# Kernel tuning notes

Hardware: AMD Instinct MI355X
Metric: run time of the kernel (lower is better)

Reference implementation:

```python
import math
import jax, jax.numpy as jnp
import numpy as np

B, H, SQ, SK, D, M = 2, 16, 2048, 2048, 128, 128

def setup_inputs() -> dict:
    key = jax.random.key(0)
    kq, kk, ks = jax.random.split(key, 3)
    q = jax.random.normal(kq, (B, H, SQ, D), dtype=jnp.float32)
    k = jax.random.normal(kk, (B, H, SK, D), dtype=jnp.float32)
    # Gaussian projection matrix S of shape (m, dim), as in generate_projection_matrix
    S = jax.random.normal(ks, (M, D), dtype=jnp.float32)
    return {"q": q, "k": k, "S": S}


def reference(q, k, S):
    """QJL: quantize keys to sign bits + norm, then asymmetric inner-product estimate.

    quantize(k):  sign_bits = sign(k @ S.T) with sign(0) -> +1;  norm_k = ||k||_2
    estimate:     <q,k> ~= <S q, sign(S k)> * (sqrt(pi/2)/m) * ||k||
    """
    m = S.shape[0]
    scale = np.float32(math.sqrt(math.pi / 2.0)) / np.float32(m)
    # --- quantize keys ---
    norm_k = jnp.linalg.norm(k, axis=-1)                      # (B,H,SK)
    proj_k = jnp.einsum('bhkd,md->bhkm', k, S)                # (B,H,SK,M)
    sign_bits = jnp.where(proj_k >= 0, 1.0, -1.0).astype(jnp.float32)
    # --- project queries (asymmetric, no quantization) ---
    Sq = jnp.einsum('bhqd,md->bhqm', q, S)                    # (B,H,SQ,M)
    # --- estimate inner products: (Sq * signs).sum(-1) for every (q, k) pair ---
    dots = jnp.einsum('bhqm,bhkm->bhqk', Sq, sign_bits)       # (B,H,SQ,SK)
    estimated = dots * scale * norm_k[:, :, None, :]
    return estimated
```

## Files before the change

kernel.cpp:

```cpp
#include <hip/hip_runtime.h>
#include <hip/hip_bf16.h>
#include <math.h>

#define NBH   32
#define SEQ   2048
#define DD    128
#define MM    128

typedef unsigned short u16;
typedef unsigned int   u32;
typedef unsigned char  u8;
typedef float  f32x4  __attribute__((ext_vector_type(4)));
typedef __bf16 bf16x8 __attribute__((ext_vector_type(8)));

#define SCALE_F 0.009791516697777346f
#define TAU 0.18f
#define CCAP 2048

static __device__ __forceinline__ u16 f2bf(float f) {
  union { float f; u32 u; } v; v.f = f;
  u32 u = v.u;
  u += 0x7fffu + ((u >> 16) & 1u);
  return (u16)(u >> 16);
}

static __device__ __forceinline__ u32 f64_negbit(const float* __restrict__ K,
                                                 const float* __restrict__ S,
                                                 int row_g, int m) {
  const f32x4* kr = (const f32x4*)(K + (size_t)row_g * DD);
  const f32x4* sr = (const f32x4*)(S + (size_t)m * DD);
  double a0 = 0, a1 = 0, a2 = 0, a3 = 0;
#pragma unroll
  for (int d = 0; d < 32; d += 4) {
    f32x4 x0 = kr[d],   y0 = sr[d];
    f32x4 x1 = kr[d+1], y1 = sr[d+1];
    f32x4 x2 = kr[d+2], y2 = sr[d+2];
    f32x4 x3 = kr[d+3], y3 = sr[d+3];
    a0 += (double)x0.x*y0.x + (double)x0.y*y0.y + (double)x0.z*y0.z + (double)x0.w*y0.w;
    a1 += (double)x1.x*y1.x + (double)x1.y*y1.y + (double)x1.z*y1.z + (double)x1.w*y1.w;
    a2 += (double)x2.x*y2.x + (double)x2.y*y2.y + (double)x2.z*y2.z + (double)x2.w*y2.w;
    a3 += (double)x3.x*y3.x + (double)x3.y*y3.y + (double)x3.z*y3.z + (double)x3.w*y3.w;
  }
  return (((a0 + a1) + (a2 + a3)) < 0.0) ? 1u : 0u;
}

static __device__ __forceinline__ void mfma_tile(const u16* lA, const u16* lB,
                                                 int wave, int lane,
                                                 f32x4 acc[4][4]) {
  const int wr = wave >> 1, wc = wave & 1;
  const int lrow = lane & 15, lkg = lane >> 4;
#pragma unroll
  for (int kk = 0; kk < 4; ++kk) {
    bf16x8 af[4], bfr[4];
    const int c = kk * 4 + lkg;
#pragma unroll
    for (int a = 0; a < 4; ++a) {
      const int r  = wr * 64 + a * 16 + lrow;
      const int r2 = wc * 64 + a * 16 + lrow;
      af[a]  = *(const bf16x8*)((const char*)lA + r  * 256 + ((c ^ (r  & 7)) << 4));
      bfr[a] = *(const bf16x8*)((const char*)lB + r2 * 256 + ((c ^ (r2 & 7)) << 4));
    }
#pragma unroll
    for (int a = 0; a < 4; ++a)
#pragma unroll
      for (int b = 0; b < 4; ++b)
        acc[a][b] = __builtin_amdgcn_mfma_f32_16x16x32_bf16(af[a], bfr[b], acc[a][b], 0, 0, 0);
  }
}

static __device__ __forceinline__ void stage_f32_to_bf16(const float* __restrict__ src,
                                                         u16* lds, int tid) {
#pragma unroll
  for (int j = 0; j < 8; ++j) {
    int i = tid + j * 256;
    int r = i >> 4, c = i & 15;
    const f32x4* gp = (const f32x4*)(src + (size_t)r * DD + c * 8);
    f32x4 v0 = gp[0], v1 = gp[1];
    union { u16 h[8]; f32x4 v; } pk;
    pk.h[0] = f2bf(v0.x); pk.h[1] = f2bf(v0.y); pk.h[2] = f2bf(v0.z); pk.h[3] = f2bf(v0.w);
    pk.h[4] = f2bf(v1.x); pk.h[5] = f2bf(v1.y); pk.h[6] = f2bf(v1.z); pk.h[7] = f2bf(v1.w);
    *(f32x4*)((char*)lds + r * 256 + ((c ^ (r & 7)) << 4)) = pk.v;
  }
}

__global__ __launch_bounds__(256) void k_proj(
    const float* __restrict__ Q, const float* __restrict__ K,
    const float* __restrict__ S, u16* __restrict__ Sqb, u8* __restrict__ Sgb,
    float* __restrict__ sn) {
  __shared__ __align__(16) u16 lds2[2 * 128 * 128];
  __shared__ u16 cbuf[CCAP];
  __shared__ u32 lcnt;
  u16* lA = lds2;
  u16* lB = lds2 + 128 * 128;
  const int tid = threadIdx.x;
  const int tile = blockIdx.x;
  const bool isK = (tile >= 512);
  const int row0 = (isK ? (tile - 512) : tile) * 128;
  const float* src = isK ? K : Q;

  if (tid == 0) lcnt = 0;

  stage_f32_to_bf16(S, lB, tid);
  stage_f32_to_bf16(src + (size_t)row0 * DD, lA, tid);

  if (isK) {
    const int row = tid >> 1, half = tid & 1;
    const f32x4* base = (const f32x4*)(src + (size_t)(row0 + row) * DD) + half * 16;
    float s = 0.f;
#pragma unroll
    for (int j = 0; j < 16; ++j) {
      f32x4 v = base[j];
      s += v.x * v.x + v.y * v.y + v.z * v.z + v.w * v.w;
    }
    s += __shfl_xor(s, 1);
    if (half == 0) sn[row0 + row] = SCALE_F * sqrtf(s);
  }
  __syncthreads();

  const int wave = tid >> 6, lane = tid & 63;
  f32x4 acc[4][4];
#pragma unroll
  for (int a = 0; a < 4; ++a)
#pragma unroll
    for (int b = 0; b < 4; ++b) acc[a][b] = (f32x4){0.f, 0.f, 0.f, 0.f};

  mfma_tile(lA, lB, wave, lane, acc);

  __syncthreads();
  float* lc = (float*)lds2;
  const int wr = wave >> 1, wc = wave & 1;
#pragma unroll
  for (int a = 0; a < 4; ++a) {
#pragma unroll
    for (int b = 0; b < 4; ++b) {
      const int col = wc * 64 + b * 16 + (lane & 15);
#pragma unroll
      for (int j = 0; j < 4; ++j) {
        const int row = wr * 64 + a * 16 + (lane >> 4) * 4 + j;
        lc[row * 128 + (col ^ (((row >> 2) & 1) << 4))] = acc[a][b][j];
      }
    }
  }
  __syncthreads();

  const int c8 = tid & 15;
  const int rr = tid >> 4;
#pragma unroll
  for (int p = 0; p < 8; ++p) {
    const int row = rr + p * 16;
    const int s = (row >> 2) & 1;
    const int cb = (c8 ^ (s << 1)) * 8;
    f32x4 v0 = *(const f32x4*)&lc[row * 128 + cb];
    f32x4 v1 = *(const f32x4*)&lc[row * 128 + cb + 4];
    float vals[8] = {v0.x, v0.y, v0.z, v0.w, v1.x, v1.y, v1.z, v1.w};
    const int row_g = row0 + row;
    if (!isK) {
      union { u16 h[8]; f32x4 v; } pk;
#pragma unroll
      for (int e = 0; e < 8; ++e) pk.h[e] = f2bf(vals[e]);
      *(f32x4*)(Sqb + (size_t)row_g * MM + c8 * 8) = pk.v;
    } else {
      u32 byteval = 0;
#pragma unroll
      for (int e = 0; e < 8; ++e) {
        const int m = c8 * 8 + e;
        u32 bitneg = (vals[e] < 0.f) ? 1u : 0u;
        if (fabsf(vals[e]) < TAU) {
          u32 pos = atomicAdd(&lcnt, 1u);
          if (pos < CCAP) cbuf[pos] = (u16)((row << 8) | (bitneg << 7) | m);
          else bitneg = f64_negbit(K, S, row_g, m);
        }
        byteval |= bitneg << e;
      }
      Sgb[(size_t)row_g * 16 + c8] = (u8)byteval;
    }
  }

  if (isK) {
    __syncthreads();
    __threadfence();
    u32 n = lcnt; if (n > CCAP) n = CCAP;
    u32* Sg32 = (u32*)Sgb;
    for (u32 i = tid; i < n; i += 256) {
      u32 code = cbuf[i];
      int r = (code >> 8) & 127, m = code & 127;
      u32 prov = (code >> 7) & 1;
      u32 f64b = f64_negbit(K, S, row0 + r, m);
      if (f64b != prov)
        atomicXor(Sg32 + (size_t)(row0 + r) * 4 + (m >> 5), 1u << (m & 31));
    }
  }
}

__global__ __launch_bounds__(256, 4) void k_gemm(
    const u16* __restrict__ Sqb, const u8* __restrict__ Sgb,
    const float* __restrict__ sn, float* __restrict__ out) {
  __shared__ __align__(16) char smem[32768 + 2048];
  const u32* lBb = (const u32*)(smem + 32768);
  const int tid = threadIdx.x;
  const u32 id = blockIdx.x;
  const u32 l = (id & 7) * 1024 + (id >> 3);
  const int tn = l & 15, tm = (l >> 4) & 15, bh = l >> 8;
  const char* Abase = (const char*)(Sqb + ((size_t)bh * SEQ + tm * 128) * MM);
  const char* Bbase = (const char*)(Sgb + ((size_t)bh * SEQ + tn * 128) * 16);

  {
    typedef __attribute__((address_space(3))) char lds_t;
    typedef const __attribute__((address_space(1))) char glob_t;
    const int wv = tid >> 6, ln = tid & 63;
#pragma unroll
    for (int j = 0; j < 8; ++j) {
      const int s = j * 256 + wv * 64 + ln;
      const int r = s >> 4, cp = s & 15;
      const int srcoff = r * 256 + ((cp ^ (r & 7)) << 4);
      __builtin_amdgcn_global_load_lds((glob_t*)(Abase + srcoff),
                                       (lds_t*)(smem + s * 16), 16, 0, 0);
    }
    if (tid < 128)
      __builtin_amdgcn_global_load_lds((glob_t*)(Bbase + tid * 16),
                                       (lds_t*)(smem + 32768 + tid * 16), 16, 0, 0);
  }
  __syncthreads();

  const int wave = tid >> 6, lane = tid & 63;
  const int wr = wave >> 1, wc = wave & 1;
  const int lrow = lane & 15, lkg = lane >> 4;
  f32x4 acc[4][4];
#pragma unroll
  for (int a = 0; a < 4; ++a)
#pragma unroll
    for (int b = 0; b < 4; ++b) acc[a][b] = (f32x4){0.f, 0.f, 0.f, 0.f};

#pragma unroll
  for (int kk = 0; kk < 4; ++kk) {
    const int c = kk * 4 + lkg;
    bf16x8 af[4], bfr[4];
#pragma unroll
    for (int a = 0; a < 4; ++a) {
      const int r = wr * 64 + a * 16 + lrow;
      af[a] = *(const bf16x8*)(smem + r * 256 + ((c ^ (r & 7)) << 4));
      const int r2 = wc * 64 + a * 16 + lrow;
      u32 word = lBb[r2 * 4 + kk];
      u32 byte = (word >> (lkg * 8)) & 0xFFu;
      union { u16 h[8]; bf16x8 v; } ub;
#pragma unroll
      for (int e = 0; e < 8; ++e) ub.h[e] = ((byte >> e) & 1u) ? 0xBF80 : 0x3F80;
      bfr[a] = ub.v;
    }
#pragma unroll
    for (int a = 0; a < 4; ++a)
#pragma unroll
      for (int b = 0; b < 4; ++b)
        acc[a][b] = __builtin_amdgcn_mfma_f32_16x16x32_bf16(af[a], bfr[b], acc[a][b], 0, 0, 0);
  }

  const float* snb = sn + bh * SEQ + tn * 128;
  const size_t outbase = (size_t)bh * SEQ * SEQ + (size_t)tm * 128 * SEQ + tn * 128;
  const int cch = tid & 31;
  const int hr0 = tid >> 5;
  const f32x4 s4 = *(const f32x4*)(snb + cch * 4);
  float* lc = (float*)smem;

#pragma unroll
  for (int h = 0; h < 2; ++h) {
    __syncthreads();
#pragma unroll
    for (int a2 = 0; a2 < 2; ++a2) {
      const int a = 2 * h + a2;
#pragma unroll
      for (int b = 0; b < 4; ++b) {
        const int col = wc * 64 + b * 16 + (lane & 15);
#pragma unroll
        for (int j = 0; j < 4; ++j) {
          const int hr = wr * 32 + a2 * 16 + (lane >> 4) * 4 + j;
          lc[hr * 128 + (col ^ (((hr >> 2) & 1) << 4))] = acc[a][b][j];
        }
      }
    }
    __syncthreads();
#pragma unroll
    for (int p = 0; p < 8; ++p) {
      const int hr = hr0 + p * 8;
      const int row = ((hr >> 5) << 6) + 32 * h + (hr & 31);
      const int cs = cch ^ (((hr >> 2) & 1) << 2);
      f32x4 v = *(const f32x4*)&lc[hr * 128 + cs * 4];
      v = v * s4;
      __builtin_nontemporal_store(v, (f32x4*)(out + outbase + (size_t)row * SEQ + cch * 4));
    }
  }
}

extern "C" void kernel_launch(void* const* d_in, const int* in_sizes, int n_in,
                              void* d_out, int out_size, void* d_ws, size_t ws_size,
                              hipStream_t stream) {
  const float* q = (const float*)d_in[0];
  const float* k = (const float*)d_in[1];
  const float* S = (const float*)d_in[2];
  float* out = (float*)d_out;
  char* ws = (char*)d_ws;

  const size_t off_Sq  = 0;
  const size_t off_Sg  = 16777216;
  const size_t off_sn  = 17825792;

  u16*   Sqb = (u16*)(ws + off_Sq);
  u8*    Sgb = (u8*)(ws + off_Sg);
  float* sn  = (float*)(ws + off_sn);

  k_proj<<<1024, 256, 0, stream>>>(q, k, S, Sqb, Sgb, sn);
  k_gemm<<<8192, 256, 0, stream>>>(Sqb, Sgb, sn, out);
}
```

Baseline: 163.0 us.

## Split projection kernel into half-M blocks with pre-converted bf16 S

```diff
diff --git a/kernel.cpp b/kernel.cpp
--- a/kernel.cpp
+++ b/kernel.cpp
@@ -2,7 +2,6 @@
 #include <hip/hip_bf16.h>
 #include <math.h>
 
-#define NBH   32
 #define SEQ   2048
 #define DD    128
 #define MM    128
@@ -15,7 +14,7 @@
 
 #define SCALE_F 0.009791516697777346f
 #define TAU 0.18f
-#define CCAP 2048
+#define CCAP 1024
 
 static __device__ __forceinline__ u16 f2bf(float f) {
   union { float f; u32 u; } v; v.f = f;
@@ -44,126 +43,119 @@
   return (((a0 + a1) + (a2 + a3)) < 0.0) ? 1u : 0u;
 }
 
-static __device__ __forceinline__ void mfma_tile(const u16* lA, const u16* lB,
-                                                 int wave, int lane,
-                                                 f32x4 acc[4][4]) {
-  const int wr = wave >> 1, wc = wave & 1;
+__global__ __launch_bounds__(256) void k_convS(const float* __restrict__ S,
+                                               u16* __restrict__ Sb) {
+  int i = blockIdx.x * 256 + threadIdx.x;
+  Sb[i] = f2bf(S[i]);
+}
+
+__global__ __launch_bounds__(256, 4) void k_proj(
+    const float* __restrict__ Q, const float* __restrict__ K,
+    const float* __restrict__ S, const u16* __restrict__ Sb,
+    u16* __restrict__ Sqb, u8* __restrict__ Sgb, float* __restrict__ sn) {
+  __shared__ __align__(16) char smem[32768];
+  __shared__ u16 cbuf[CCAP];
+  __shared__ u32 lcnt;
+  const int tid = threadIdx.x;
+  const u32 id = blockIdx.x;
+  const int mhalf = id & 1;
+  const bool isK = (id >> 1) & 1;
+  const int row0 = (int)(id >> 2) * 128;
+  const int col0 = mhalf * 64;
+  const float* src = isK ? K : Q;
+
+  if (tid == 0) lcnt = 0;
+
+  {
+    const bool donorm = isK && (mhalf == 0);
+#pragma unroll
+    for (int j = 0; j < 8; ++j) {
+      const int i = tid + j * 256;
+      const int r = i >> 4, c = i & 15;
+      const f32x4* gp = (const f32x4*)(src + (size_t)(row0 + r) * DD + c * 8);
+      f32x4 v0 = gp[0], v1 = gp[1];
+      union { u16 h[8]; f32x4 v; } pk;
+      pk.h[0] = f2bf(v0.x); pk.h[1] = f2bf(v0.y); pk.h[2] = f2bf(v0.z); pk.h[3] = f2bf(v0.w);
+      pk.h[4] = f2bf(v1.x); pk.h[5] = f2bf(v1.y); pk.h[6] = f2bf(v1.z); pk.h[7] = f2bf(v1.w);
+      *(f32x4*)(smem + r * 256 + ((c ^ (r & 7)) << 4)) = pk.v;
+      if (donorm) {
+        float ss = v0.x*v0.x + v0.y*v0.y + v0.z*v0.z + v0.w*v0.w
+                 + v1.x*v1.x + v1.y*v1.y + v1.z*v1.z + v1.w*v1.w;
+        ss += __shfl_xor(ss, 1); ss += __shfl_xor(ss, 2);
+        ss += __shfl_xor(ss, 4); ss += __shfl_xor(ss, 8);
+        if ((tid & 15) == 0) sn[row0 + r] = SCALE_F * sqrtf(ss);
+      }
+    }
+  }
+  __syncthreads();
+
+  const int wave = tid >> 6, lane = tid & 63;
   const int lrow = lane & 15, lkg = lane >> 4;
+  f32x4 acc[2][4];
+#pragma unroll
+  for (int a = 0; a < 2; ++a)
+#pragma unroll
+    for (int b = 0; b < 4; ++b) acc[a][b] = (f32x4){0.f, 0.f, 0.f, 0.f};
+
+  const char* Sbb = (const char*)Sb;
 #pragma unroll
   for (int kk = 0; kk < 4; ++kk) {
-    bf16x8 af[4], bfr[4];
     const int c = kk * 4 + lkg;
-#pragma unroll
-    for (int a = 0; a < 4; ++a) {
-      const int r  = wr * 64 + a * 16 + lrow;
-      const int r2 = wc * 64 + a * 16 + lrow;
-      af[a]  = *(const bf16x8*)((const char*)lA + r  * 256 + ((c ^ (r  & 7)) << 4));
-      bfr[a] = *(const bf16x8*)((const char*)lB + r2 * 256 + ((c ^ (r2 & 7)) << 4));
-    }
-#pragma unroll
-    for (int a = 0; a < 4; ++a)
+    bf16x8 af[2], bfr[4];
+#pragma unroll
+    for (int a = 0; a < 2; ++a) {
+      const int r = wave * 32 + a * 16 + lrow;
+      af[a] = *(const bf16x8*)(smem + r * 256 + ((c ^ (r & 7)) << 4));
+    }
+#pragma unroll
+    for (int b = 0; b < 4; ++b) {
+      const int r2 = col0 + b * 16 + lrow;
+      bfr[b] = *(const bf16x8*)(Sbb + (size_t)r2 * 256 + c * 16);
+    }
+#pragma unroll
+    for (int a = 0; a < 2; ++a)
 #pragma unroll
       for (int b = 0; b < 4; ++b)
         acc[a][b] = __builtin_amdgcn_mfma_f32_16x16x32_bf16(af[a], bfr[b], acc[a][b], 0, 0, 0);
   }
-}
-
-static __device__ __forceinline__ void stage_f32_to_bf16(const float* __restrict__ src,
-                                                         u16* lds, int tid) {
-#pragma unroll
-  for (int j = 0; j < 8; ++j) {
-    int i = tid + j * 256;
-    int r = i >> 4, c = i & 15;
-    const f32x4* gp = (const f32x4*)(src + (size_t)r * DD + c * 8);
-    f32x4 v0 = gp[0], v1 = gp[1];
-    union { u16 h[8]; f32x4 v; } pk;
-    pk.h[0] = f2bf(v0.x); pk.h[1] = f2bf(v0.y); pk.h[2] = f2bf(v0.z); pk.h[3] = f2bf(v0.w);
-    pk.h[4] = f2bf(v1.x); pk.h[5] = f2bf(v1.y); pk.h[6] = f2bf(v1.z); pk.h[7] = f2bf(v1.w);
-    *(f32x4*)((char*)lds + r * 256 + ((c ^ (r & 7)) << 4)) = pk.v;
-  }
-}
-
-__global__ __launch_bounds__(256) void k_proj(
-    const float* __restrict__ Q, const float* __restrict__ K,
-    const float* __restrict__ S, u16* __restrict__ Sqb, u8* __restrict__ Sgb,
-    float* __restrict__ sn) {
-  __shared__ __align__(16) u16 lds2[2 * 128 * 128];
-  __shared__ u16 cbuf[CCAP];
-  __shared__ u32 lcnt;
-  u16* lA = lds2;
-  u16* lB = lds2 + 128 * 128;
-  const int tid = threadIdx.x;
-  const int tile = blockIdx.x;
-  const bool isK = (tile >= 512);
-  const int row0 = (isK ? (tile - 512) : tile) * 128;
-  const float* src = isK ? K : Q;
-
-  if (tid == 0) lcnt = 0;
-
-  stage_f32_to_bf16(S, lB, tid);
-  stage_f32_to_bf16(src + (size_t)row0 * DD, lA, tid);
-
-  if (isK) {
-    const int row = tid >> 1, half = tid & 1;
-    const f32x4* base = (const f32x4*)(src + (size_t)(row0 + row) * DD) + half * 16;
-    float s = 0.f;
-#pragma unroll
-    for (int j = 0; j < 16; ++j) {
-      f32x4 v = base[j];
-      s += v.x * v.x + v.y * v.y + v.z * v.z + v.w * v.w;
-    }
-    s += __shfl_xor(s, 1);
-    if (half == 0) sn[row0 + row] = SCALE_F * sqrtf(s);
-  }
+
   __syncthreads();
-
-  const int wave = tid >> 6, lane = tid & 63;
-  f32x4 acc[4][4];
-#pragma unroll
-  for (int a = 0; a < 4; ++a)
-#pragma unroll
-    for (int b = 0; b < 4; ++b) acc[a][b] = (f32x4){0.f, 0.f, 0.f, 0.f};
-
-  mfma_tile(lA, lB, wave, lane, acc);
-
+  float* lc = (float*)smem;
+#pragma unroll
+  for (int a = 0; a < 2; ++a) {
+#pragma unroll
+    for (int b = 0; b < 4; ++b) {
+      const int col = b * 16 + (lane & 15);
+#pragma unroll
+      for (int j = 0; j < 4; ++j) {
+        const int row = wave * 32 + a * 16 + (lane >> 4) * 4 + j;
+        lc[row * 64 + (col ^ (((row >> 2) & 3) << 4))] = acc[a][b][j];
+      }
+    }
+  }
   __syncthreads();
-  float* lc = (float*)lds2;
-  const int wr = wave >> 1, wc = wave & 1;
-#pragma unroll
-  for (int a = 0; a < 4; ++a) {
-#pragma unroll
-    for (int b = 0; b < 4; ++b) {
-      const int col = wc * 64 + b * 16 + (lane & 15);
-#pragma unroll
-      for (int j = 0; j < 4; ++j) {
-        const int row = wr * 64 + a * 16 + (lane >> 4) * 4 + j;
-        lc[row * 128 + (col ^ (((row >> 2) & 1) << 4))] = acc[a][b][j];
-      }
-    }
-  }
-  __syncthreads();
-
-  const int c8 = tid & 15;
-  const int rr = tid >> 4;
-#pragma unroll
-  for (int p = 0; p < 8; ++p) {
-    const int row = rr + p * 16;
-    const int s = (row >> 2) & 1;
-    const int cb = (c8 ^ (s << 1)) * 8;
-    f32x4 v0 = *(const f32x4*)&lc[row * 128 + cb];
-    f32x4 v1 = *(const f32x4*)&lc[row * 128 + cb + 4];
+
+#pragma unroll
+  for (int it = 0; it < 4; ++it) {
+    const int ch = tid + it * 256;
+    const int row = ch >> 3, co = ch & 7;
+    const int sw = (row >> 2) & 3;
+    const int cq0 = (co * 2) ^ (sw << 2);
+    const int cq1 = (co * 2 + 1) ^ (sw << 2);
+    f32x4 v0 = *(const f32x4*)&lc[row * 64 + cq0 * 4];
+    f32x4 v1 = *(const f32x4*)&lc[row * 64 + cq1 * 4];
     float vals[8] = {v0.x, v0.y, v0.z, v0.w, v1.x, v1.y, v1.z, v1.w};
     const int row_g = row0 + row;
     if (!isK) {
       union { u16 h[8]; f32x4 v; } pk;
 #pragma unroll
       for (int e = 0; e < 8; ++e) pk.h[e] = f2bf(vals[e]);
-      *(f32x4*)(Sqb + (size_t)row_g * MM + c8 * 8) = pk.v;
+      *(f32x4*)(Sqb + (size_t)row_g * MM + col0 + co * 8) = pk.v;
     } else {
       u32 byteval = 0;
 #pragma unroll
       for (int e = 0; e < 8; ++e) {
-        const int m = c8 * 8 + e;
+        const int m = col0 + co * 8 + e;
         u32 bitneg = (vals[e] < 0.f) ? 1u : 0u;
         if (fabsf(vals[e]) < TAU) {
           u32 pos = atomicAdd(&lcnt, 1u);
@@ -172,7 +164,7 @@
         }
         byteval |= bitneg << e;
       }
-      Sgb[(size_t)row_g * 16 + c8] = (u8)byteval;
+      Sgb[(size_t)row_g * 16 + (col0 >> 3) + co] = (u8)byteval;
     }
   }
 
@@ -302,11 +294,14 @@
   const size_t off_Sq  = 0;
   const size_t off_Sg  = 16777216;
   const size_t off_sn  = 17825792;
+  const size_t off_Sb  = 18087936;
 
   u16*   Sqb = (u16*)(ws + off_Sq);
   u8*    Sgb = (u8*)(ws + off_Sg);
   float* sn  = (float*)(ws + off_sn);
-
-  k_proj<<<1024, 256, 0, stream>>>(q, k, S, Sqb, Sgb, sn);
+  u16*   Sb  = (u16*)(ws + off_Sb);
+
+  k_convS<<<64, 256, 0, stream>>>(S, Sb);
+  k_proj<<<2048, 256, 0, stream>>>(q, k, S, Sb, Sqb, Sgb, sn);
   k_gemm<<<8192, 256, 0, stream>>>(Sqb, Sgb, sn, out);
 }
```

After: 301.5 us. 85.0% more time.

## Prepack S into MFMA fragment layout and halve k_proj LDS footprint

Applied to the files above, without the earlier changes.

```diff
diff --git a/kernel.cpp b/kernel.cpp
--- a/kernel.cpp
+++ b/kernel.cpp
@@ -44,30 +44,6 @@
   return (((a0 + a1) + (a2 + a3)) < 0.0) ? 1u : 0u;
 }
 
-static __device__ __forceinline__ void mfma_tile(const u16* lA, const u16* lB,
-                                                 int wave, int lane,
-                                                 f32x4 acc[4][4]) {
-  const int wr = wave >> 1, wc = wave & 1;
-  const int lrow = lane & 15, lkg = lane >> 4;
-#pragma unroll
-  for (int kk = 0; kk < 4; ++kk) {
-    bf16x8 af[4], bfr[4];
-    const int c = kk * 4 + lkg;
-#pragma unroll
-    for (int a = 0; a < 4; ++a) {
-      const int r  = wr * 64 + a * 16 + lrow;
-      const int r2 = wc * 64 + a * 16 + lrow;
-      af[a]  = *(const bf16x8*)((const char*)lA + r  * 256 + ((c ^ (r  & 7)) << 4));
-      bfr[a] = *(const bf16x8*)((const char*)lB + r2 * 256 + ((c ^ (r2 & 7)) << 4));
-    }
-#pragma unroll
-    for (int a = 0; a < 4; ++a)
-#pragma unroll
-      for (int b = 0; b < 4; ++b)
-        acc[a][b] = __builtin_amdgcn_mfma_f32_16x16x32_bf16(af[a], bfr[b], acc[a][b], 0, 0, 0);
-  }
-}
-
 static __device__ __forceinline__ void stage_f32_to_bf16(const float* __restrict__ src,
                                                          u16* lds, int tid) {
 #pragma unroll
@@ -83,15 +59,27 @@
   }
 }
 
+__global__ __launch_bounds__(256) void k_packS(const float* __restrict__ S,
+                                               u16* __restrict__ Sf) {
+  const int b = blockIdx.x;
+  const int tid = threadIdx.x;
+  const int kk = tid >> 6, lane = tid & 63;
+  const int rl = lane & 15, g = lane >> 4;
+  const f32x4* gp = (const f32x4*)(S + (size_t)(b * 16 + rl) * DD + kk * 32 + g * 8);
+  f32x4 v0 = gp[0], v1 = gp[1];
+  union { u16 h[8]; f32x4 v; } pk;
+  pk.h[0] = f2bf(v0.x); pk.h[1] = f2bf(v0.y); pk.h[2] = f2bf(v0.z); pk.h[3] = f2bf(v0.w);
+  pk.h[4] = f2bf(v1.x); pk.h[5] = f2bf(v1.y); pk.h[6] = f2bf(v1.z); pk.h[7] = f2bf(v1.w);
+  *(f32x4*)(Sf + ((size_t)(b * 4 + kk) * 64 + lane) * 8) = pk.v;
+}
+
 __global__ __launch_bounds__(256) void k_proj(
     const float* __restrict__ Q, const float* __restrict__ K,
-    const float* __restrict__ S, u16* __restrict__ Sqb, u8* __restrict__ Sgb,
-    float* __restrict__ sn) {
-  __shared__ __align__(16) u16 lds2[2 * 128 * 128];
+    const float* __restrict__ S, const u16* __restrict__ Sf,
+    u16* __restrict__ Sqb, u8* __restrict__ Sgb, float* __restrict__ sn) {
+  __shared__ __align__(16) u16 lA[128 * 128];
   __shared__ u16 cbuf[CCAP];
   __shared__ u32 lcnt;
-  u16* lA = lds2;
-  u16* lB = lds2 + 128 * 128;
   const int tid = threadIdx.x;
   const int tile = blockIdx.x;
   const bool isK = (tile >= 512);
@@ -100,7 +88,6 @@
 
   if (tid == 0) lcnt = 0;
 
-  stage_f32_to_bf16(S, lB, tid);
   stage_f32_to_bf16(src + (size_t)row0 * DD, lA, tid);
 
   if (isK) {
@@ -118,61 +105,82 @@
   __syncthreads();
 
   const int wave = tid >> 6, lane = tid & 63;
+  const int wr = wave >> 1, wc = wave & 1;
+  const int lrow = lane & 15, lkg = lane >> 4;
   f32x4 acc[4][4];
 #pragma unroll
   for (int a = 0; a < 4; ++a)
 #pragma unroll
     for (int b = 0; b < 4; ++b) acc[a][b] = (f32x4){0.f, 0.f, 0.f, 0.f};
 
-  mfma_tile(lA, lB, wave, lane, acc);
-
-  __syncthreads();
-  float* lc = (float*)lds2;
-  const int wr = wave >> 1, wc = wave & 1;
-#pragma unroll
-  for (int a = 0; a < 4; ++a) {
-#pragma unroll
-    for (int b = 0; b < 4; ++b) {
-      const int col = wc * 64 + b * 16 + (lane & 15);
-#pragma unroll
-      for (int j = 0; j < 4; ++j) {
-        const int row = wr * 64 + a * 16 + (lane >> 4) * 4 + j;
-        lc[row * 128 + (col ^ (((row >> 2) & 1) << 4))] = acc[a][b][j];
+#pragma unroll
+  for (int kk = 0; kk < 4; ++kk) {
+    const int c = kk * 4 + lkg;
+    bf16x8 af[4], bfr[4];
+#pragma unroll
+    for (int a = 0; a < 4; ++a) {
+      const int r = wr * 64 + a * 16 + lrow;
+      af[a] = *(const bf16x8*)((const char*)lA + r * 256 + ((c ^ (r & 7)) << 4));
+    }
+#pragma unroll
+    for (int b = 0; b < 4; ++b)
+      bfr[b] = *(const bf16x8*)(Sf + ((size_t)((wc * 4 + b) * 4 + kk) * 64 + lane) * 8);
+#pragma unroll
+    for (int a = 0; a < 4; ++a)
+#pragma unroll
+      for (int b = 0; b < 4; ++b)
+        acc[a][b] = __builtin_amdgcn_mfma_f32_16x16x32_bf16(af[a], bfr[b], acc[a][b], 0, 0, 0);
+  }
+
+  float* lc = (float*)lA;
+#pragma unroll
+  for (int h = 0; h < 2; ++h) {
+    __syncthreads();
+#pragma unroll
+    for (int a2 = 0; a2 < 2; ++a2) {
+      const int a = 2 * h + a2;
+#pragma unroll
+      for (int b = 0; b < 4; ++b) {
+        const int col = wc * 64 + b * 16 + (lane & 15);
+#pragma unroll
+        for (int j = 0; j < 4; ++j) {
+          const int hr = wr * 32 + a2 * 16 + (lane >> 4) * 4 + j;
+          lc[hr * 128 + (col ^ (((hr >> 2) & 1) << 4))] = acc[a][b][j];
+        }
       }
     }
-  }
-  __syncthreads();
-
-  const int c8 = tid & 15;
-  const int rr = tid >> 4;
-#pragma unroll
-  for (int p = 0; p < 8; ++p) {
-    const int row = rr + p * 16;
-    const int s = (row >> 2) & 1;
-    const int cb = (c8 ^ (s << 1)) * 8;
-    f32x4 v0 = *(const f32x4*)&lc[row * 128 + cb];
-    f32x4 v1 = *(const f32x4*)&lc[row * 128 + cb + 4];
-    float vals[8] = {v0.x, v0.y, v0.z, v0.w, v1.x, v1.y, v1.z, v1.w};
-    const int row_g = row0 + row;
-    if (!isK) {
-      union { u16 h[8]; f32x4 v; } pk;
-#pragma unroll
-      for (int e = 0; e < 8; ++e) pk.h[e] = f2bf(vals[e]);
-      *(f32x4*)(Sqb + (size_t)row_g * MM + c8 * 8) = pk.v;
-    } else {
-      u32 byteval = 0;
-#pragma unroll
-      for (int e = 0; e < 8; ++e) {
-        const int m = c8 * 8 + e;
-        u32 bitneg = (vals[e] < 0.f) ? 1u : 0u;
-        if (fabsf(vals[e]) < TAU) {
-          u32 pos = atomicAdd(&lcnt, 1u);
-          if (pos < CCAP) cbuf[pos] = (u16)((row << 8) | (bitneg << 7) | m);
-          else bitneg = f64_negbit(K, S, row_g, m);
+    __syncthreads();
+#pragma unroll
+    for (int it = 0; it < 4; ++it) {
+      const int ch = tid + it * 256;
+      const int hrow = ch >> 4, c8 = ch & 15;
+      const int s = (hrow >> 2) & 1;
+      const int cb = (c8 ^ (s << 1)) * 8;
+      f32x4 v0 = *(const f32x4*)&lc[hrow * 128 + cb];
+      f32x4 v1 = *(const f32x4*)&lc[hrow * 128 + cb + 4];
+      float vals[8] = {v0.x, v0.y, v0.z, v0.w, v1.x, v1.y, v1.z, v1.w};
+      const int rloc = ((hrow >> 5) << 6) + 32 * h + (hrow & 31);
+      const int row_g = row0 + rloc;
+      if (!isK) {
+        union { u16 h8[8]; f32x4 v; } pk;
+#pragma unroll
+        for (int e = 0; e < 8; ++e) pk.h8[e] = f2bf(vals[e]);
+        *(f32x4*)(Sqb + (size_t)row_g * MM + c8 * 8) = pk.v;
+      } else {
+        u32 byteval = 0;
+#pragma unroll
+        for (int e = 0; e < 8; ++e) {
+          const int m = c8 * 8 + e;
+          u32 bitneg = (vals[e] < 0.f) ? 1u : 0u;
+          if (fabsf(vals[e]) < TAU) {
+            u32 pos = atomicAdd(&lcnt, 1u);
+            if (pos < CCAP) cbuf[pos] = (u16)((rloc << 8) | (bitneg << 7) | m);
+            else bitneg = f64_negbit(K, S, row_g, m);
+          }
+          byteval |= bitneg << e;
         }
-        byteval |= bitneg << e;
+        Sgb[(size_t)row_g * 16 + c8] = (u8)byteval;
       }
-      Sgb[(size_t)row_g * 16 + c8] = (u8)byteval;
     }
   }
 
@@ -302,11 +310,14 @@
   const size_t off_Sq  = 0;
   const size_t off_Sg  = 16777216;
   const size_t off_sn  = 17825792;
+  const size_t off_Sf  = 18087936;
 
   u16*   Sqb = (u16*)(ws + off_Sq);
   u8*    Sgb = (u8*)(ws + off_Sg);
   float* sn  = (float*)(ws + off_sn);
-
-  k_proj<<<1024, 256, 0, stream>>>(q, k, S, Sqb, Sgb, sn);
+  u16*   Sf  = (u16*)(ws + off_Sf);
+
+  k_packS<<<8, 256, 0, stream>>>(S, Sf);
+  k_proj<<<1024, 256, 0, stream>>>(q, k, S, Sf, Sqb, Sgb, sn);
   k_gemm<<<8192, 256, 0, stream>>>(Sqb, Sgb, sn, out);
 }
```

Result: slower. 201.9 us (+23.9%).
